# Kernel optimization log

Hardware: AMD Instinct MI355X
Metric: run time of the kernel (lower is better)

## Reference

```python
import jax, jax.numpy as jnp
import numpy as np

RADIUS = 0.2
N_POINT = 1024   # FPS centroids
N_SAMPLE = 64    # ball-query neighbors


def swish(x):
    return x * jax.nn.sigmoid(x)


def farthest_point_sample(xyz, npoint):
    # xyz: [B, N, 3] -> [B, npoint] int32 indices (deterministic: start = arange(B) % N)
    B, N, _ = xyz.shape
    batch = jnp.arange(B)

    def step(carry, _):
        distance, farthest = carry
        centroid = xyz[batch, farthest][:, None, :]            # [B,1,3]
        dist = jnp.sum((xyz - centroid) ** 2, axis=-1)          # [B,N]
        distance = jnp.minimum(distance, dist)
        nxt = jnp.argmax(distance, axis=-1).astype(jnp.int32)
        return (distance, nxt), farthest

    init = (jnp.full((B, N), 1e10, dtype=xyz.dtype),
            (jnp.arange(B, dtype=jnp.int32) % N))
    _, idx = jax.lax.scan(step, init, None, length=npoint)      # [npoint, B]
    return idx.T                                                # [B, npoint]


def square_distance(src, dst):
    # src [B,S,3], dst [B,N,3] -> [B,S,N]
    return (jnp.sum(src ** 2, -1)[:, :, None]
            + jnp.sum(dst ** 2, -1)[:, None, :]
            - 2.0 * jnp.einsum('bsc,bnc->bsn', src, dst))


def query_ball_point(radius, nsample, xyz, new_xyz):
    # xyz [B,N,3], new_xyz [B,S,3] -> [B,S,nsample] int32
    N = xyz.shape[1]
    sqrdists = square_distance(new_xyz, xyz)                     # [B,S,N]
    arange_n = jnp.arange(N, dtype=jnp.int32)
    group_idx = jnp.where(sqrdists > radius ** 2, N, arange_n[None, None, :])
    group_idx = jnp.sort(group_idx, axis=-1)[:, :, :nsample]     # [B,S,K]
    first = group_idx[:, :, :1]
    return jnp.where(group_idx == N, first, group_idx).astype(jnp.int32)


def index_points(points, idx):
    # points [B,N,C], idx [B,...] -> [B,...,C]
    return jax.vmap(lambda p, i: p[i])(points, idx)


def setup_inputs() -> dict:
    key = jax.random.key(0)
    k1, k2, k3, k4 = jax.random.split(key, 4)
    B, N, D = 4, 16384, 256
    c_in = D + 3  # 259
    xyz = jax.random.normal(k1, (B, 3, N), dtype=jnp.float32)
    points = jax.random.normal(k2, (B, D, N), dtype=jnp.float32)
    w1 = jax.random.normal(k3, (512, c_in), dtype=jnp.float32) / np.sqrt(c_in)
    b1 = jnp.zeros((512,), dtype=jnp.float32)
    w2 = jax.random.normal(k4, (512, 512), dtype=jnp.float32) / np.sqrt(512)
    b2 = jnp.zeros((512,), dtype=jnp.float32)
    return {"xyz": xyz, "points": points, "w1": w1, "b1": b1, "w2": w2, "b2": b2}


def reference(xyz, points, w1, b1, w2, b2):
    x = jnp.transpose(xyz, (0, 2, 1))        # [B,N,3]
    p = jnp.transpose(points, (0, 2, 1))     # [B,N,D]

    fps_idx = farthest_point_sample(x, N_POINT)                  # [B,S]
    new_xyz = index_points(x, fps_idx)                           # [B,S,3]
    idx = query_ball_point(RADIUS, N_SAMPLE, x, new_xyz)         # [B,S,K]
    grouped_xyz = index_points(x, idx)                           # [B,S,K,3]
    grouped_norm = grouped_xyz - new_xyz[:, :, None, :]
    grouped_pts = index_points(p, idx)                           # [B,S,K,D]
    feat = jnp.concatenate([grouped_norm, grouped_pts], axis=-1) # [B,S,K,3+D]

    h = jnp.transpose(feat, (0, 3, 2, 1))                        # [B,C,K,S]
    # 1x1 convs (patch_size=1) == per-position channel GEMM
    h = swish(jnp.einsum('bcks,oc->boks', h, w1) + b1[None, :, None, None])
    h = swish(jnp.einsum('bcks,oc->boks', h, w2) + b2[None, :, None, None])
    return jnp.mean(h, axis=2)                                   # [B,512,S]
```

## Files before the change

kernel.cpp:

```cpp
#include <hip/hip_runtime.h>
#include <hip/hip_bf16.h>
#include <stdint.h>

#define BB 4
#define NN 16384
#define SS 1024
#define KSAMP 64
#define DD 256
#define CIN 259
#define HH 512
#define R2C 0.04f

#define OFF_PTS  0ull
#define OFF_Q    33554432ull
#define OFF_W1P  33816576ull
#define OFF_W2P  34111488ull
#define OFF_CX   34635776ull
#define OFF_CY   34652160ull
#define OFF_CZ   34668544ull
#define OFF_PROG 34684928ull

typedef __attribute__((ext_vector_type(8))) short bf16x8;
typedef __attribute__((ext_vector_type(4))) short bf16x4;
typedef __attribute__((ext_vector_type(4))) float f32x4;

__device__ __forceinline__ unsigned short f2bf(float f) {
    unsigned u = __float_as_uint(f);
    u = u + 0x7fffu + ((u >> 16) & 1u);
    return (unsigned short)(u >> 16);
}

__global__ __launch_bounds__(1024) void k_prep2(const float* __restrict__ xyz,
                                                const float* __restrict__ pts,
                                                const float* __restrict__ w1,
                                                const float* __restrict__ w2,
                                                unsigned char* __restrict__ ws)
{
    __shared__ __align__(16) unsigned char smem[64 * 264 * 2];
    const int blk = blockIdx.x;
    const int t   = threadIdx.x;

    if (blk < 1024) {
        const int b  = blk >> 8;
        const int n0 = (blk & 255) << 6;
        unsigned short* sT = (unsigned short*)smem;
        const int tn = t & 63, tc = t >> 6;
        for (int cc = tc; cc < 256; cc += 16) {
            float v = pts[((size_t)(b * 256 + cc)) * NN + n0 + tn];
            sT[tn * 264 + cc] = f2bf(v);
        }
        __syncthreads();
        unsigned short* ptsT = (unsigned short*)(ws + OFF_PTS);
        const int r = t >> 4, part = t & 15;
        size_t ob = (((size_t)b * NN) + n0 + r) * 256 + part * 16;
        bf16x8* dst = (bf16x8*)(ptsT + ob);
        const bf16x8* src = (const bf16x8*)(sT + r * 264 + part * 16);
        dst[0] = src[0];
        dst[1] = src[1];
    } else if (blk < 1088) {
        const int qb = blk - 1024;
        const int b = qb >> 4;
        const int n = ((qb & 15) << 10) + t;
        const float* xb = xyz + (size_t)b * 3 * NN;
        float X = xb[n], Y = xb[NN + n], Z = xb[2 * NN + n];
        float q = __fadd_rn(__fadd_rn(__fmul_rn(X, X), __fmul_rn(Y, Y)), __fmul_rn(Z, Z));
        ((float*)(ws + OFF_Q))[b * NN + n] = q;
    } else if (blk == 1088) {
        unsigned short* w1p = (unsigned short*)(ws + OFF_W1P);
        for (int e = t; e < 32 * 9 * 64 * 8; e += 1024) {
            int j = e & 7, lane = (e >> 3) & 63, rest = e >> 9;
            int kt = rest % 9, nt = rest / 9;
            int kk = kt * 32 + 4 * (lane >> 4) + (j & 3) + 16 * (j >> 2);
            int o  = nt * 16 + (lane & 15);
            float v = 0.f;
            if (kk < CIN) {
                int c = (kk < 256) ? (kk + 3) : (kk - 256);
                v = w1[o * CIN + c];
            }
            w1p[e] = f2bf(v);
        }
    } else {
        unsigned short* w2p = (unsigned short*)(ws + OFF_W2P);
        for (int e = t; e < 32 * 16 * 64 * 8; e += 1024) {
            int j = e & 7, lane = (e >> 3) & 63, rest = e >> 9;
            int kt = rest & 15, nt = rest >> 4;
            int kk = kt * 32 + 4 * (lane >> 4) + (j & 3) + 16 * (j >> 2);
            int o  = nt * 16 + (lane & 15);
            w2p[e] = f2bf(w2[o * 512 + kk]);
        }
    }
}

__global__ __launch_bounds__(1024) void k_fused(const float* __restrict__ xyz,
                                                const float* __restrict__ b1,
                                                const float* __restrict__ b2,
                                                unsigned char* __restrict__ ws,
                                                float* __restrict__ out)
{
    __shared__ __align__(16) unsigned char smem[104832];
    const int blk = blockIdx.x;
    const int t   = threadIdx.x;
    int* prog = (int*)(ws + OFF_PROG);
    float* cxs = (float*)(ws + OFF_CX);
    float* cys = (float*)(ws + OFF_CY);
    float* czs = (float*)(ws + OFF_CZ);

    if (blk < 4) {
        const int b = blk;
        const float* xb = xyz + (size_t)b * 3 * NN;
        float x[16], y[16], z[16], d[16];
        const int base = t * 16;
        const float4* xv = (const float4*)(xb + base);
        const float4* yv = (const float4*)(xb + NN + base);
        const float4* zv = (const float4*)(xb + 2 * NN + base);
#pragma unroll
        for (int i = 0; i < 4; i++) {
            float4 a = xv[i]; x[4*i]=a.x; x[4*i+1]=a.y; x[4*i+2]=a.z; x[4*i+3]=a.w;
            float4 c = yv[i]; y[4*i]=c.x; y[4*i+1]=c.y; y[4*i+2]=c.z; y[4*i+3]=c.w;
            float4 e = zv[i]; z[4*i]=e.x; z[4*i+1]=e.y; z[4*i+2]=e.z; z[4*i+3]=e.w;
        }
#pragma unroll
        for (int i = 0; i < 16; i++) d[i] = 1e10f;

        float* sC    = (float*)smem;
        float* sWMax = (float*)smem + 4;
        int*   sWin  = (int*)((float*)smem + 20);

        if (t == (b >> 4)) {
#pragma unroll
            for (int k = 0; k < 16; k++)
                if ((b & 15) == k) { sC[0] = x[k]; sC[1] = y[k]; sC[2] = z[k]; }
        }
        __syncthreads();

        for (int it = 0; it < SS; ++it) {
            const float cx = sC[0], cy = sC[1], cz = sC[2];
            if (t == 0) {
                __hip_atomic_store(&cxs[(b << 10) + it], cx, __ATOMIC_RELAXED,
                                   __HIP_MEMORY_SCOPE_AGENT);
                __hip_atomic_store(&cys[(b << 10) + it], cy, __ATOMIC_RELAXED,
                                   __HIP_MEMORY_SCOPE_AGENT);
                __hip_atomic_store(&czs[(b << 10) + it], cz, __ATOMIC_RELAXED,
                                   __HIP_MEMORY_SCOPE_AGENT);
                if ((it & 7) == 0)
                    __hip_atomic_store(&prog[b], it, __ATOMIC_RELEASE,
                                       __HIP_MEMORY_SCOPE_AGENT);
                *sWin = 0x7fffffff;
            }
            if (it == SS - 1) break;

            float bl = -1.0f;
#pragma unroll
            for (int k = 0; k < 16; k++) {
                float dx = __fsub_rn(x[k], cx);
                float dy = __fsub_rn(y[k], cy);
                float dz = __fsub_rn(z[k], cz);
                float s  = __fadd_rn(__fadd_rn(__fmul_rn(dx, dx), __fmul_rn(dy, dy)),
                                     __fmul_rn(dz, dz));
                float nd = fminf(d[k], s);
                d[k] = nd;
                bl = fmaxf(bl, nd);
            }
            float bm = bl;
#pragma unroll
            for (int off = 32; off; off >>= 1) bm = fmaxf(bm, __shfl_xor(bm, off));
            if ((t & 63) == 0) sWMax[t >> 6] = bm;
            __syncthreads();

            float gm = sWMax[0];
#pragma unroll
            for (int wv = 1; wv < 16; wv++) gm = fmaxf(gm, sWMax[wv]);

            if (bl == gm) {
                int cand = 0x7fffffff;
#pragma unroll
                for (int k = 15; k >= 0; k--) if (d[k] == gm) cand = base + k;
                atomicMin(sWin, cand);
            }
            __syncthreads();
            const int w = *sWin;
            if (t == (w >> 4)) {
                const int wk = w & 15;
#pragma unroll
                for (int k = 0; k < 16; k++)
                    if (wk == k) { sC[0] = x[k]; sC[1] = y[k]; sC[2] = z[k]; }
            }
            __syncthreads();
        }
        if (t == 0)
            __hip_atomic_store(&prog[b], SS, __ATOMIC_RELEASE,
                               __HIP_MEMORY_SCOPE_AGENT);
        return;
    }

    const int i = blk - 4;
    const int b = i & 3, s = i >> 2;
    const int cs = (b << 10) + s;

    unsigned short* sFeat = (unsigned short*)smem;
    unsigned short* sH1   = (unsigned short*)(smem + 37888);
    int*            sIdx  = (int*)(smem + 104448);

    if (t == 0) {
        while (__hip_atomic_load(&prog[b], __ATOMIC_ACQUIRE,
                                 __HIP_MEMORY_SCOPE_AGENT) <= s)
            __builtin_amdgcn_s_sleep(8);
    }
    __syncthreads();

    const float cx = __hip_atomic_load(&cxs[cs], __ATOMIC_RELAXED,
                                       __HIP_MEMORY_SCOPE_AGENT);
    const float cy = __hip_atomic_load(&cys[cs], __ATOMIC_RELAXED,
                                       __HIP_MEMORY_SCOPE_AGENT);
    const float cz = __hip_atomic_load(&czs[cs], __ATOMIC_RELAXED,
                                       __HIP_MEMORY_SCOPE_AGENT);
    const float* xb = xyz + (size_t)b * 3 * NN;

    if (t < 64) {
        const int lane = t;
        const float* Q = (const float*)(ws + OFF_Q) + b * NN;
        const float qc = __fadd_rn(__fadd_rn(__fmul_rn(cx, cx), __fmul_rn(cy, cy)),
                                   __fmul_rn(cz, cz));
        int collected = 0;
        int first = -1;
        for (int c = 0; c < 256; c++) {
            const int n = (c << 6) + lane;
            float px = xb[n], py = xb[NN + n], pz = xb[2 * NN + n], qj = Q[n];
            float dot = __fadd_rn(__fadd_rn(__fmul_rn(cx, px), __fmul_rn(cy, py)),
                                  __fmul_rn(cz, pz));
            float r = __fsub_rn(__fadd_rn(qc, qj), __fmul_rn(2.0f, dot));
            bool valid = !(r > R2C);
            unsigned long long m = __ballot(valid);
            if (m) {
                if (first < 0) first = (c << 6) + __builtin_ctzll(m);
                int rank = __popcll(m & ((1ull << lane) - 1ull));
                int slot = collected + rank;
                if (valid && slot < 64) sIdx[slot] = n;
                collected += __popcll(m);
                if (collected >= 64) break;
            }
        }
        if (collected < 64) {
            for (int k = collected + lane; k < 64; k += 64) sIdx[k] = first;
        }
    }
    __syncthreads();

    {
        const unsigned short* ptsT = (const unsigned short*)(ws + OFF_PTS);
        const int k = t >> 4, part = t & 15;
        const int n = sIdx[k];
        const bf16x8* src = (const bf16x8*)(ptsT + ((size_t)b * NN + n) * 256 + part * 16);
        bf16x8* dst = (bf16x8*)(sFeat + k * 296 + part * 16);
        dst[0] = src[0];
        dst[1] = src[1];
    }
    if (t < 64) {
        const int n = sIdx[t];
        sFeat[t * 296 + 256] = f2bf(__fsub_rn(xb[n], cx));
        sFeat[t * 296 + 257] = f2bf(__fsub_rn(xb[NN + n], cy));
        sFeat[t * 296 + 258] = f2bf(__fsub_rn(xb[2 * NN + n], cz));
#pragma unroll
        for (int c = 259; c < 288; c++) sFeat[t * 296 + c] = 0;
    }
    __syncthreads();

    const int wv = t >> 6, lane = t & 63;
    const int l15 = lane & 15, g = lane >> 4;

    f32x4 acc[4][2];
#pragma unroll
    for (int a = 0; a < 4; a++)
#pragma unroll
        for (int j = 0; j < 2; j++) acc[a][j] = (f32x4){0.f, 0.f, 0.f, 0.f};

    const bf16x8* w1v = (const bf16x8*)(ws + OFF_W1P);
    for (int kt = 0; kt < 9; kt++) {
        bf16x8 af[4];
#pragma unroll
        for (int mt = 0; mt < 4; mt++) {
            const unsigned short* p = sFeat + (mt * 16 + l15) * 296 + kt * 32 + 4 * g;
            bf16x4 lo = *(const bf16x4*)p;
            bf16x4 hi = *(const bf16x4*)(p + 16);
            af[mt] = __builtin_shufflevector(lo, hi, 0, 1, 2, 3, 4, 5, 6, 7);
        }
        bf16x8 bfr[2];
#pragma unroll
        for (int nti = 0; nti < 2; nti++)
            bfr[nti] = w1v[((wv * 2 + nti) * 9 + kt) * 64 + lane];
#pragma unroll
        for (int mt = 0; mt < 4; mt++)
#pragma unroll
            for (int nti = 0; nti < 2; nti++)
                acc[mt][nti] = __builtin_amdgcn_mfma_f32_16x16x32_bf16(
                    af[mt], bfr[nti], acc[mt][nti], 0, 0, 0);
    }
#pragma unroll
    for (int mt = 0; mt < 4; mt++)
#pragma unroll
        for (int nti = 0; nti < 2; nti++) {
            const int o = (wv * 2 + nti) * 16 + l15;
            const float bias = b1[o];
#pragma unroll
            for (int r = 0; r < 4; r++) {
                float v = acc[mt][nti][r] + bias;
                float sw = v / (1.f + __expf(-v));
                sH1[(mt * 16 + g * 4 + r) * 520 + o] = f2bf(sw);
            }
        }
    __syncthreads();

#pragma unroll
    for (int a = 0; a < 4; a++)
#pragma unroll
        for (int j = 0; j < 2; j++) acc[a][j] = (f32x4){0.f, 0.f, 0.f, 0.f};

    const bf16x8* w2v = (const bf16x8*)(ws + OFF_W2P);
    for (int kt = 0; kt < 16; kt++) {
        bf16x8 af[4];
#pragma unroll
        for (int mt = 0; mt < 4; mt++) {
            const unsigned short* p = sH1 + (mt * 16 + l15) * 520 + kt * 32 + 4 * g;
            bf16x4 lo = *(const bf16x4*)p;
            bf16x4 hi = *(const bf16x4*)(p + 16);
            af[mt] = __builtin_shufflevector(lo, hi, 0, 1, 2, 3, 4, 5, 6, 7);
        }
        bf16x8 bfr[2];
#pragma unroll
        for (int nti = 0; nti < 2; nti++)
            bfr[nti] = w2v[((wv * 2 + nti) * 16 + kt) * 64 + lane];
#pragma unroll
        for (int mt = 0; mt < 4; mt++)
#pragma unroll
            for (int nti = 0; nti < 2; nti++)
                acc[mt][nti] = __builtin_amdgcn_mfma_f32_16x16x32_bf16(
                    af[mt], bfr[nti], acc[mt][nti], 0, 0, 0);
    }
#pragma unroll
    for (int nti = 0; nti < 2; nti++) {
        float tot = 0.f;
        const int o = (wv * 2 + nti) * 16 + l15;
        const float bias = b2[o];
#pragma unroll
        for (int mt = 0; mt < 4; mt++) {
#pragma unroll
            for (int r = 0; r < 4; r++) {
                float v = acc[mt][nti][r] + bias;
                tot += v / (1.f + __expf(-v));
            }
        }
        tot += __shfl_xor(tot, 16);
        tot += __shfl_xor(tot, 32);
        if (lane < 16) {
            const int oo = (wv * 2 + nti) * 16 + lane;
            out[((size_t)b * 512 + oo) * 1024 + s] = tot * 0.015625f;
        }
    }
}

extern "C" void kernel_launch(void* const* d_in, const int* in_sizes, int n_in,
                              void* d_out, int out_size, void* d_ws, size_t ws_size,
                              hipStream_t stream)
{
    const float* xyz = (const float*)d_in[0];
    const float* pts = (const float*)d_in[1];
    const float* w1  = (const float*)d_in[2];
    const float* b1  = (const float*)d_in[3];
    const float* w2  = (const float*)d_in[4];
    const float* b2  = (const float*)d_in[5];
    float* out = (float*)d_out;
    unsigned char* ws = (unsigned char*)d_ws;

    hipMemsetAsync((void*)(ws + OFF_PROG), 0xFF, 16, stream);
    k_prep2<<<1090, 1024, 0, stream>>>(xyz, pts, w1, w2, ws);
    k_fused<<<4100, 1024, 0, stream>>>(xyz, b1, b2, ws, out);
}
```

Baseline: 1.647 ms.

## Use packed argmax keys and a single barrier per FPS iteration

```diff
diff --git a/kernel.cpp b/kernel.cpp
--- a/kernel.cpp
+++ b/kernel.cpp
@@ -97,7 +97,7 @@
                                                 unsigned char* __restrict__ ws,
                                                 float* __restrict__ out)
 {
-    __shared__ __align__(16) unsigned char smem[104832];
+    __shared__ __align__(16) unsigned char smem[131328];
     const int blk = blockIdx.x;
     const int t   = threadIdx.x;
     int* prog = (int*)(ws + OFF_PROG);
@@ -106,35 +106,27 @@
     float* czs = (float*)(ws + OFF_CZ);
 
     if (blk < 4) {
+#pragma clang fp contract(off)
         const int b = blk;
         const float* xb = xyz + (size_t)b * 3 * NN;
-        float x[16], y[16], z[16], d[16];
-        const int base = t * 16;
-        const float4* xv = (const float4*)(xb + base);
-        const float4* yv = (const float4*)(xb + NN + base);
-        const float4* zv = (const float4*)(xb + 2 * NN + base);
-#pragma unroll
-        for (int i = 0; i < 4; i++) {
-            float4 a = xv[i]; x[4*i]=a.x; x[4*i+1]=a.y; x[4*i+2]=a.z; x[4*i+3]=a.w;
-            float4 c = yv[i]; y[4*i]=c.x; y[4*i+1]=c.y; y[4*i+2]=c.z; y[4*i+3]=c.w;
-            float4 e = zv[i]; z[4*i]=e.x; z[4*i+1]=e.y; z[4*i+2]=e.z; z[4*i+3]=e.w;
-        }
-#pragma unroll
-        for (int i = 0; i < 16; i++) d[i] = 1e10f;
-
-        float* sC    = (float*)smem;
-        float* sWMax = (float*)smem + 4;
-        int*   sWin  = (int*)((float*)smem + 20);
-
-        if (t == (b >> 4)) {
-#pragma unroll
-            for (int k = 0; k < 16; k++)
-                if ((b & 15) == k) { sC[0] = x[k]; sC[1] = y[k]; sC[2] = z[k]; }
-        }
+        float* sXY = (float*)smem;
+        unsigned long long* sK = (unsigned long long*)(smem + 131072);
+
+        float z[16], d[16];
+#pragma unroll
+        for (int k = 0; k < 16; k++) {
+            const int n = (k << 10) + t;
+            float X = xb[n], Y = xb[NN + n];
+            z[k] = xb[2 * NN + n];
+            d[k] = 1e10f;
+            sXY[2 * n]     = X;
+            sXY[2 * n + 1] = Y;
+        }
+        const int wv = t >> 6, lane = t & 63;
+        float cx = xb[b], cy = xb[NN + b], cz = xb[2 * NN + b];
         __syncthreads();
 
         for (int it = 0; it < SS; ++it) {
-            const float cx = sC[0], cy = sC[1], cz = sC[2];
             if (t == 0) {
                 __hip_atomic_store(&cxs[(b << 10) + it], cx, __ATOMIC_RELAXED,
                                    __HIP_MEMORY_SCOPE_AGENT);
@@ -145,47 +137,44 @@
                 if ((it & 7) == 0)
                     __hip_atomic_store(&prog[b], it, __ATOMIC_RELEASE,
                                        __HIP_MEMORY_SCOPE_AGENT);
-                *sWin = 0x7fffffff;
             }
             if (it == SS - 1) break;
 
             float bl = -1.0f;
+            int   bk = 0;
 #pragma unroll
             for (int k = 0; k < 16; k++) {
-                float dx = __fsub_rn(x[k], cx);
-                float dy = __fsub_rn(y[k], cy);
+                const float2 xy = *(const float2*)(sXY + 2 * ((k << 10) + t));
+                float dx = __fsub_rn(xy.x, cx);
+                float dy = __fsub_rn(xy.y, cy);
                 float dz = __fsub_rn(z[k], cz);
                 float s  = __fadd_rn(__fadd_rn(__fmul_rn(dx, dx), __fmul_rn(dy, dy)),
                                      __fmul_rn(dz, dz));
                 float nd = fminf(d[k], s);
                 d[k] = nd;
-                bl = fmaxf(bl, nd);
-            }
-            float bm = bl;
-#pragma unroll
-            for (int off = 32; off; off >>= 1) bm = fmaxf(bm, __shfl_xor(bm, off));
-            if ((t & 63) == 0) sWMax[t >> 6] = bm;
+                if (nd > bl) { bl = nd; bk = k; }
+            }
+            const int bi = (bk << 10) + t;
+            unsigned long long key =
+                ((unsigned long long)__float_as_uint(bl) << 32) |
+                (unsigned)(0xFFFFFFFFu - (unsigned)bi);
+#pragma unroll
+            for (int off = 1; off < 64; off <<= 1) {
+                unsigned long long o = __shfl_xor(key, off);
+                if (o > key) key = o;
+            }
+            if (lane == 0) sK[((it & 1) << 4) + wv] = key;
             __syncthreads();
 
-            float gm = sWMax[0];
-#pragma unroll
-            for (int wv = 1; wv < 16; wv++) gm = fmaxf(gm, sWMax[wv]);
-
-            if (bl == gm) {
-                int cand = 0x7fffffff;
-#pragma unroll
-                for (int k = 15; k >= 0; k--) if (d[k] == gm) cand = base + k;
-                atomicMin(sWin, cand);
-            }
-            __syncthreads();
-            const int w = *sWin;
-            if (t == (w >> 4)) {
-                const int wk = w & 15;
-#pragma unroll
-                for (int k = 0; k < 16; k++)
-                    if (wk == k) { sC[0] = x[k]; sC[1] = y[k]; sC[2] = z[k]; }
-            }
-            __syncthreads();
+            unsigned long long gk = sK[((it & 1) << 4) + (lane & 15)];
+#pragma unroll
+            for (int off = 1; off < 16; off <<= 1) {
+                unsigned long long o = __shfl_xor(gk, off);
+                if (o > gk) gk = o;
+            }
+            const int widx = __builtin_amdgcn_readfirstlane(
+                (int)(0xFFFFFFFFu - (unsigned)gk));
+            cx = xb[widx]; cy = xb[NN + widx]; cz = xb[2 * NN + widx];
         }
         if (t == 0)
             __hip_atomic_store(&prog[b], SS, __ATOMIC_RELEASE,
```

Result: slower. 2.245 ms (+36.3%).
